# Performance work log

Measured on AMD Instinct MI355X. Metric: run time of the kernel, lower is better.

## Reference

```python
import jax, jax.numpy as jnp
import numpy as np

B, N, D = 1024, 8192, 128
BETA = 0.25


def setup_inputs() -> dict:
    key = jax.random.key(0)
    kx, kw = jax.random.split(key)
    x = jax.random.normal(kx, (B, D), dtype=jnp.float32)
    # nn.Embedding weight init: uniform(-1/num_embeddings, 1/num_embeddings)
    W = jax.random.uniform(kw, (N, D), dtype=jnp.float32, minval=-1.0 / N, maxval=1.0 / N)
    return {"x": x, "W": W}


def reference(x, W):
    # Squared L2 distances: (B, N) via expansion; single GEMM for the cross term.
    dist = (x * x).sum(axis=1, keepdims=True) - 2.0 * (x @ W.T) + (W * W).sum(axis=1)[None, :]
    # (-dist).topk(k=1) == argmin(dist); torch keeps the k dim -> ind is (B, 1)
    ind = jnp.argmin(dist, axis=1)[:, None]
    q = W[ind]  # (B, 1, D) codebook gather (matches torch embedding(ind) shape)
    # Faithful to source: (B, D) broadcasts against (B, 1, D) -> (B, B, D)
    loss = BETA * jnp.mean((x - jax.lax.stop_gradient(q)) ** 2) + jnp.mean((jax.lax.stop_gradient(x) - q) ** 2)
    quantized = x + jax.lax.stop_gradient(q - x)  # straight-through; (B, B, D) per source broadcast
    return quantized, ind, loss
```

## Files before the change

### kernel.cpp

```cpp
#include <hip/hip_runtime.h>
#include <stdint.h>

typedef float vfloat4 __attribute__((ext_vector_type(4)));

static const long long QN       = 134217728LL;
static const long long IND_OFF  = QN;
static const long long LOSS_OFF = QN + 1024;

#define WS_W2    0
#define WS_X2    8192
#define WS_SX    9216
#define WS_IND   9344
#define WS_PVAL  16384
#define WS_PIDX  81920
#define WS_Q     147456

__global__ __launch_bounds__(256) void k_prep(const float* __restrict__ x,
                                              const float* __restrict__ W,
                                              float* __restrict__ ws) {
    const int b = blockIdx.x, tid = threadIdx.x;
    if (b < 36) {
        const float4* pr = (b < 32) ? ((const float4*)W + (size_t)(b * 256 + tid) * 32)
                                    : ((const float4*)x + (size_t)((b - 32) * 256 + tid) * 32);
        float s = 0.0f;
#pragma unroll 8
        for (int t = 0; t < 32; ++t) {
            float4 v = pr[t];
            s += v.x * v.x + v.y * v.y + v.z * v.z + v.w * v.w;
        }
        if (b < 32) ws[WS_W2 + b * 256 + tid] = s;
        else        ws[WS_X2 + (b - 32) * 256 + tid] = s;
    } else {
        __shared__ float sh[8][32];
        const int c = tid & 31, g = tid >> 5;
        const int col = (b - 36) * 32 + c;
        float sum = 0.0f;
        for (int r = g; r < 1024; r += 8) sum += x[(size_t)r * 128 + col];
        sh[g][c] = sum;
        __syncthreads();
        if (g == 0) {
            float t = 0.0f;
#pragma unroll
            for (int gg = 0; gg < 8; ++gg) t += sh[gg][c];
            ws[WS_SX + col] = t;
        }
    }
}

__global__ __launch_bounds__(256) void k_score(
    const float* __restrict__ x, const float* __restrict__ W,
    const float* __restrict__ w2, const float* __restrict__ x2,
    float* __restrict__ pval, int* __restrict__ pidx) {
    __shared__ float Xs[32][132];
    __shared__ float Wst[32][132];
    const int tid = threadIdx.x;
    const int tx = tid & 15, ty = tid >> 4;
    const int n0 = blockIdx.x * 128, m0 = blockIdx.y * 128;
    const float4* xv = (const float4*)x;
    const float4* wv = (const float4*)W;

    float acc[8][8];
#pragma unroll
    for (int i = 0; i < 8; ++i)
#pragma unroll
        for (int j = 0; j < 8; ++j) acc[i][j] = 0.0f;

    for (int kc = 0; kc < 4; ++kc) {
#pragma unroll
        for (int it = 0; it < 4; ++it) {
            int f = it * 256 + tid;
            int m = f >> 3, kq = f & 7;
            float4 a = xv[(size_t)(m0 + m) * 32 + kc * 8 + kq];
            float4 b = wv[(size_t)(n0 + m) * 32 + kc * 8 + kq];
            Xs[kq * 4 + 0][m] = a.x;
            Xs[kq * 4 + 1][m] = a.y;
            Xs[kq * 4 + 2][m] = a.z;
            Xs[kq * 4 + 3][m] = a.w;
            Wst[kq * 4 + 0][m] = b.x;
            Wst[kq * 4 + 1][m] = b.y;
            Wst[kq * 4 + 2][m] = b.z;
            Wst[kq * 4 + 3][m] = b.w;
        }
        __syncthreads();
#pragma unroll 8
        for (int k = 0; k < 32; ++k) {
            float4 a0 = *(const float4*)&Xs[k][ty * 8];
            float4 a1 = *(const float4*)&Xs[k][ty * 8 + 4];
            float4 b0 = *(const float4*)&Wst[k][tx * 8];
            float4 b1 = *(const float4*)&Wst[k][tx * 8 + 4];
            float af[8] = {a0.x, a0.y, a0.z, a0.w, a1.x, a1.y, a1.z, a1.w};
            float bf[8] = {b0.x, b0.y, b0.z, b0.w, b1.x, b1.y, b1.z, b1.w};
#pragma unroll
            for (int i = 0; i < 8; ++i)
#pragma unroll
                for (int j = 0; j < 8; ++j) acc[i][j] += af[i] * bf[j];
        }
        __syncthreads();
    }

    float w2v[8];
#pragma unroll
    for (int j = 0; j < 8; ++j) w2v[j] = w2[n0 + tx * 8 + j];

#pragma unroll
    for (int i = 0; i < 8; ++i) {
        const int row = m0 + ty * 8 + i;
        const float xxv = x2[row];
        float bestv;
        int besti = n0 + tx * 8;
        {
            float t = xxv - 2.0f * acc[i][0];
            bestv = t + w2v[0];
        }
#pragma unroll
        for (int j = 1; j < 8; ++j) {
            float t = xxv - 2.0f * acc[i][j];
            float s = t + w2v[j];
            if (s < bestv) { bestv = s; besti = n0 + tx * 8 + j; }
        }
        for (int off = 1; off < 16; off <<= 1) {
            float ov = __shfl_xor(bestv, off, 64);
            int oi = __shfl_xor(besti, off, 64);
            if (ov < bestv || (ov == bestv && oi < besti)) { bestv = ov; besti = oi; }
        }
        if (tx == 0) {
            pval[row * 64 + blockIdx.x] = bestv;
            pidx[row * 64 + blockIdx.x] = besti;
        }
    }
}

__global__ __launch_bounds__(128) void k_argmin(
    const float* __restrict__ W,
    const float* __restrict__ pval, const int* __restrict__ pidx,
    float* __restrict__ out, float* __restrict__ ws) {
    const int tid = threadIdx.x;
    const int w = tid >> 6, lane = tid & 63;
    const int r = blockIdx.x * 2 + w;
    float bestv = pval[r * 64 + lane];
    int besti = pidx[r * 64 + lane];
    for (int off = 1; off < 64; off <<= 1) {
        float ov = __shfl_xor(bestv, off, 64);
        int oi = __shfl_xor(besti, off, 64);
        if (ov < bestv || (ov == bestv && oi < besti)) { bestv = ov; besti = oi; }
    }
    if (lane == 0) {
        out[IND_OFF + r] = (float)besti;
        ((int*)ws)[WS_IND + r] = besti;
    }
    if (lane < 32) {
        const float4* wv = (const float4*)W;
        float4* wsq = (float4*)(ws + WS_Q);
        wsq[(size_t)r * 32 + lane] = wv[(size_t)besti * 32 + lane];
    }
}

__global__ __launch_bounds__(256) void k_bcast(float* __restrict__ out,
                                               const float* __restrict__ ws) {
    const int bid = blockIdx.x, tid = threadIdx.x;
    if (bid == 0) {
        __shared__ float shq[2][128];
        __shared__ float sh[256];
        const int d = tid & 127, g = tid >> 7;
        float s = 0.0f;
        for (int r = g; r < 1024; r += 2) s += ws[WS_Q + (size_t)r * 128 + d];
        shq[g][d] = s;
        __syncthreads();
        float dotv = 0.0f;
        if (tid < 128) dotv = (shq[0][tid] + shq[1][tid]) * ws[WS_SX + tid];
        float sx2 = 0.0f;
        for (int r = tid; r < 1024; r += 256) sx2 += ws[WS_X2 + r];
        const int* wsI = (const int*)ws + WS_IND;
        float sq2 = 0.0f;
        for (int r = tid; r < 1024; r += 256) sq2 += ws[WS_W2 + wsI[r]];
        sh[tid] = dotv;
        __syncthreads();
        for (int st = 128; st > 0; st >>= 1) {
            if (tid < st) sh[tid] += sh[tid + st];
            __syncthreads();
        }
        const float dot = sh[0];
        __syncthreads();
        sh[tid] = sx2;
        __syncthreads();
        for (int st = 128; st > 0; st >>= 1) {
            if (tid < st) sh[tid] += sh[tid + st];
            __syncthreads();
        }
        const float Sx2 = sh[0];
        __syncthreads();
        sh[tid] = sq2;
        __syncthreads();
        for (int st = 128; st > 0; st >>= 1) {
            if (tid < st) sh[tid] += sh[tid + st];
            __syncthreads();
        }
        if (tid == 0) {
            double loss = 1.25 * (1024.0 * (double)Sx2 + 1024.0 * (double)sh[0] - 2.0 * (double)dot) / 134217728.0;
            out[LOSS_OFF] = (float)loss;
        }
        __syncthreads();
    }
    const int i = bid >> 3;
    const int e = bid & 7;
    const int t = tid & 31;
    const vfloat4* src = (const vfloat4*)(ws + WS_Q) + (size_t)i * 32;
    vfloat4 qv = src[t];
    vfloat4* dst = (vfloat4*)out + (size_t)i * 32768 + t;
    const int jend = e * 128 + 128;
    for (int j = e * 128 + (tid >> 5); j < jend; j += 8) {
        dst[(size_t)j * 32] = qv;
    }
}

extern "C" void kernel_launch(void* const* d_in, const int* in_sizes, int n_in,
                              void* d_out, int out_size, void* d_ws, size_t ws_size,
                              hipStream_t stream) {
    const float* x = (const float*)d_in[0];
    const float* W = (const float*)d_in[1];
    float* out = (float*)d_out;
    float* ws = (float*)d_ws;

    hipLaunchKernelGGL(k_prep, dim3(40), dim3(256), 0, stream, x, W, ws);
    hipLaunchKernelGGL(k_score, dim3(64, 8), dim3(256), 0, stream, x, W,
                       ws + WS_W2, ws + WS_X2, ws + WS_PVAL, (int*)(ws + WS_PIDX));
    hipLaunchKernelGGL(k_argmin, dim3(512), dim3(128), 0, stream, W,
                       ws + WS_PVAL, (const int*)(ws + WS_PIDX), out, ws);
    hipLaunchKernelGGL(k_bcast, dim3(8192), dim3(256), 0, stream, out, ws);
}
```

Before: 729.7 us.

## Fuse argmin reduction into broadcast kernel and use nontemporal stores

Removes the separate argmin kernel: each broadcast block now reduces the 64 partial minima for its row itself, gathers the codebook row into shared memory, and writes the broadcast output with nontemporal stores. Block 0 also recomputes all 1024 argmins serially in order to evaluate the loss after its broadcast work, instead of reading a staged workspace. The scoring loop unroll drops from 8 to 4. The fusion saves one launch and a workspace round trip, but every row's argmin is now recomputed by 8 blocks, and block 0 becomes a long serial tail. Block 0's serial scan keeps only strict improvements, so on exact ties it picks the first partial rather than the smallest index.

```diff
diff --git a/kernel.cpp b/kernel.cpp
--- a/kernel.cpp
+++ b/kernel.cpp
@@ -10,10 +10,8 @@
 #define WS_W2    0
 #define WS_X2    8192
 #define WS_SX    9216
-#define WS_IND   9344
 #define WS_PVAL  16384
 #define WS_PIDX  81920
-#define WS_Q     147456
 
 __global__ __launch_bounds__(256) void k_prep(const float* __restrict__ x,
                                               const float* __restrict__ W,
@@ -82,7 +80,7 @@
             Wst[kq * 4 + 3][m] = b.w;
         }
         __syncthreads();
-#pragma unroll 8
+#pragma unroll 4
         for (int k = 0; k < 32; ++k) {
             float4 a0 = *(const float4*)&Xs[k][ty * 8];
             float4 a1 = *(const float4*)&Xs[k][ty * 8 + 4];
@@ -130,49 +128,68 @@
     }
 }
 
-__global__ __launch_bounds__(128) void k_argmin(
+__global__ __launch_bounds__(256) void k_bcast(
     const float* __restrict__ W,
     const float* __restrict__ pval, const int* __restrict__ pidx,
-    float* __restrict__ out, float* __restrict__ ws) {
-    const int tid = threadIdx.x;
-    const int w = tid >> 6, lane = tid & 63;
-    const int r = blockIdx.x * 2 + w;
-    float bestv = pval[r * 64 + lane];
-    int besti = pidx[r * 64 + lane];
-    for (int off = 1; off < 64; off <<= 1) {
-        float ov = __shfl_xor(bestv, off, 64);
-        int oi = __shfl_xor(besti, off, 64);
-        if (ov < bestv || (ov == bestv && oi < besti)) { bestv = ov; besti = oi; }
-    }
-    if (lane == 0) {
-        out[IND_OFF + r] = (float)besti;
-        ((int*)ws)[WS_IND + r] = besti;
-    }
-    if (lane < 32) {
-        const float4* wv = (const float4*)W;
-        float4* wsq = (float4*)(ws + WS_Q);
-        wsq[(size_t)r * 32 + lane] = wv[(size_t)besti * 32 + lane];
-    }
-}
-
-__global__ __launch_bounds__(256) void k_bcast(float* __restrict__ out,
-                                               const float* __restrict__ ws) {
+    float* __restrict__ out, const float* __restrict__ ws) {
     const int bid = blockIdx.x, tid = threadIdx.x;
+    const int i = bid >> 3;
+    const int e = bid & 7;
+    __shared__ float qrow[128];
+    __shared__ int sbesti;
+    if (tid < 64) {
+        float bestv = pval[i * 64 + tid];
+        int besti = pidx[i * 64 + tid];
+        for (int off = 1; off < 64; off <<= 1) {
+            float ov = __shfl_xor(bestv, off, 64);
+            int oi = __shfl_xor(besti, off, 64);
+            if (ov < bestv || (ov == bestv && oi < besti)) { bestv = ov; besti = oi; }
+        }
+        if (tid == 0) {
+            sbesti = besti;
+            if (e == 0) out[IND_OFF + i] = (float)besti;
+        }
+    }
+    __syncthreads();
+    const int idx = sbesti;
+    if (tid < 32) ((float4*)qrow)[tid] = ((const float4*)W)[(size_t)idx * 32 + tid];
+    __syncthreads();
+
+    const int t = tid & 31;
+    vfloat4 qv = ((const vfloat4*)qrow)[t];
+    vfloat4* dst = (vfloat4*)out + (size_t)i * 32768 + t;
+    const int jend = e * 128 + 128;
+    for (int j = e * 128 + (tid >> 5); j < jend; j += 8) {
+        __builtin_nontemporal_store(qv, &dst[(size_t)j * 32]);
+    }
+
     if (bid == 0) {
-        __shared__ float shq[2][128];
+        __shared__ int sind[1024];
+        __shared__ float shd[2][128];
         __shared__ float sh[256];
+#pragma unroll
+        for (int rr = 0; rr < 4; ++rr) {
+            const int r = rr * 256 + tid;
+            float bv = pval[r * 64];
+            int bi = pidx[r * 64];
+            for (int c = 1; c < 64; ++c) {
+                float v = pval[r * 64 + c];
+                if (v < bv) { bv = v; bi = pidx[r * 64 + c]; }
+            }
+            sind[r] = bi;
+        }
+        __syncthreads();
         const int d = tid & 127, g = tid >> 7;
         float s = 0.0f;
-        for (int r = g; r < 1024; r += 2) s += ws[WS_Q + (size_t)r * 128 + d];
-        shq[g][d] = s;
-        __syncthreads();
-        float dotv = 0.0f;
-        if (tid < 128) dotv = (shq[0][tid] + shq[1][tid]) * ws[WS_SX + tid];
-        float sx2 = 0.0f;
-        for (int r = tid; r < 1024; r += 256) sx2 += ws[WS_X2 + r];
-        const int* wsI = (const int*)ws + WS_IND;
-        float sq2 = 0.0f;
-        for (int r = tid; r < 1024; r += 256) sq2 += ws[WS_W2 + wsI[r]];
+        for (int r = g; r < 1024; r += 2) s += W[(size_t)sind[r] * 128 + d];
+        shd[g][d] = s;
+        __syncthreads();
+        float dotv = (tid < 128) ? (shd[0][tid] + shd[1][tid]) * ws[WS_SX + tid] : 0.0f;
+        float sx2 = 0.0f, sq2 = 0.0f;
+        for (int r = tid; r < 1024; r += 256) {
+            sx2 += ws[WS_X2 + r];
+            sq2 += ws[WS_W2 + sind[r]];
+        }
         sh[tid] = dotv;
         __syncthreads();
         for (int st = 128; st > 0; st >>= 1) {
@@ -199,17 +216,6 @@
             double loss = 1.25 * (1024.0 * (double)Sx2 + 1024.0 * (double)sh[0] - 2.0 * (double)dot) / 134217728.0;
             out[LOSS_OFF] = (float)loss;
         }
-        __syncthreads();
-    }
-    const int i = bid >> 3;
-    const int e = bid & 7;
-    const int t = tid & 31;
-    const vfloat4* src = (const vfloat4*)(ws + WS_Q) + (size_t)i * 32;
-    vfloat4 qv = src[t];
-    vfloat4* dst = (vfloat4*)out + (size_t)i * 32768 + t;
-    const int jend = e * 128 + 128;
-    for (int j = e * 128 + (tid >> 5); j < jend; j += 8) {
-        dst[(size_t)j * 32] = qv;
     }
 }
 
@@ -224,7 +230,6 @@
     hipLaunchKernelGGL(k_prep, dim3(40), dim3(256), 0, stream, x, W, ws);
     hipLaunchKernelGGL(k_score, dim3(64, 8), dim3(256), 0, stream, x, W,
                        ws + WS_W2, ws + WS_X2, ws + WS_PVAL, (int*)(ws + WS_PIDX));
-    hipLaunchKernelGGL(k_argmin, dim3(512), dim3(128), 0, stream, W,
-                       ws + WS_PVAL, (const int*)(ws + WS_PIDX), out, ws);
-    hipLaunchKernelGGL(k_bcast, dim3(8192), dim3(256), 0, stream, out, ws);
-}
+    hipLaunchKernelGGL(k_bcast, dim3(8192), dim3(256), 0, stream,
+                       W, ws + WS_PVAL, (const int*)(ws + WS_PIDX), out, ws);
+}
```

After: 672.8 us. -7.8%, faster.
